# Performance work log

Hardware: AMD Instinct MI355X
Metric: run time of the kernel (lower is better)

The kernel has to match this reference:

```python
import jax, jax.numpy as jnp
import numpy as np

NUM_USERS = 1_000_000
EMBED_DIM = 64
N_NODES = 16384
K = 50
NEG_INF = -1e30


def setup_inputs() -> dict:
    key = jax.random.key(0)
    ks = jax.random.split(key, 7)
    d = EMBED_DIM
    table = jax.random.normal(ks[0], (NUM_USERS, d), jnp.float32) * 0.02
    nodes = jax.random.randint(ks[1], (N_NODES,), 0, NUM_USERS)
    neigh_idx = jax.random.randint(ks[2], (N_NODES, K), 0, NUM_USERS)
    neigh_mask = jax.random.randint(ks[3], (N_NODES, K), 0, 2).astype(bool)
    neigh_mask = neigh_mask.at[:, 0].set(True)  # every node has >=1 neighbor
    W1 = jax.random.normal(ks[4], (2 * d, d), jnp.float32) / np.sqrt(2 * d)
    b1 = jnp.zeros((d,), jnp.float32)
    W2 = jax.random.normal(ks[5], (d, d), jnp.float32) / np.sqrt(d)
    b2 = jnp.zeros((d,), jnp.float32)
    W3 = jax.random.normal(ks[6], (d, 1), jnp.float32) / np.sqrt(d)
    b3 = jnp.zeros((1,), jnp.float32)
    return dict(table=table, W1=W1, b1=b1, W2=W2, b2=b2, W3=W3, b3=b3,
                nodes=nodes, neigh_idx=neigh_idx, neigh_mask=neigh_mask)


def reference(table, W1, b1, W2, b2, W3, b3, nodes, neigh_idx, neigh_mask):
    # Gather neighbor embeddings and center-node embeddings (eval mode: dropout off).
    E = table[neigh_idx]                                   # [N, K, d]
    U = table[nodes]                                       # [N, d]
    Uk = jnp.broadcast_to(U[:, None, :], E.shape)          # [N, K, d]
    x = jnp.concatenate([E, Uk], axis=-1)                  # [N, K, 2d]
    h = jax.nn.relu(x @ W1 + b1)                           # [N, K, d]
    h = jax.nn.relu(h @ W2 + b2)                           # [N, K, d]
    s = (h @ W3 + b3)[..., 0]                              # [N, K]
    # Masked softmax over the ragged neighbor dimension.
    s = jnp.where(neigh_mask, s, NEG_INF)
    att = jax.nn.softmax(s, axis=-1)                       # [N, K]
    # Attention-weighted sum of neighbor embeddings: e_u.T @ att_w per node.
    out = jnp.einsum('nk,nkd->nd', att, E)                 # [N, d]
    return out
```

## Files before the change

### kernel.cpp

```cpp
#include <hip/hip_runtime.h>
#include <hip/hip_bf16.h>

#define NN 16384
#define KK 50
#define DD 64

typedef __attribute__((ext_vector_type(8))) short bf16x8;
typedef __attribute__((ext_vector_type(4))) float f32x4;

__device__ __forceinline__ float bf2f(unsigned short u) {
    union { unsigned int i; float f; } v;
    v.i = ((unsigned int)u) << 16;
    return v.f;
}
__device__ __forceinline__ unsigned short f2bf(float f) {
    union { float f; unsigned int i; } v; v.f = f;
    unsigned int lsb = (v.i >> 16) & 1u;
    v.i += 0x7fffu + lsb;
    return (unsigned short)(v.i >> 16);
}

template<int BF16>
__device__ __forceinline__ float ldv(const void* p, size_t i) {
    if (BF16) return bf2f(((const unsigned short*)p)[i]);
    else      return ((const float*)p)[i];
}

template<int BF16>
__device__ __forceinline__ bf16x8 load8(const void* p, size_t off) {
    if (BF16) {
        return *(const bf16x8*)((const unsigned short*)p + off);
    } else {
        const float* f = (const float*)p + off;
        bf16x8 r;
#pragma unroll
        for (int j = 0; j < 8; ++j) ((unsigned short*)&r)[j] = f2bf(f[j]);
        return r;
    }
}

__global__ void prep_kernel(const unsigned int* __restrict__ tw,
                            const unsigned int* __restrict__ mw,
                            const void* __restrict__ W1_,
                            const void* __restrict__ W2_,
                            int* __restrict__ flags,
                            unsigned short* __restrict__ W1top,
                            unsigned short* __restrict__ W1bot,
                            unsigned short* __restrict__ W2p) {
    __shared__ int sflags[2];
    const int t = threadIdx.x;
    if (t < 64) {
        const unsigned int w  = tw[t];
        const unsigned int lo = w & 0xFFFFu;
        const unsigned int ex = (lo >> 7) & 0xFFu;
        const bool bf_like = (ex >= 96u && ex <= 126u);
        const unsigned long long bb = __ballot(bf_like);
        bool found = false;
#pragma unroll
        for (int i = 0; i < 8; ++i) found |= (mw[t + i * 64] > 1u);
        const unsigned long long mb = __ballot(found);
        if (t == 0) {
            sflags[0] = (mb != 0ull) ? 1 : 0;
            sflags[1] = (__popcll(bb) >= 48) ? 1 : 0;
            flags[0] = sflags[0];
            flags[1] = sflags[1];
        }
    }
    __syncthreads();
    const int bf = sflags[1];
    {
        const int f = t >> 6, lane = t & 63;
        const int kt = f >> 2, nt = f & 3;
        const int q = lane >> 4, col = lane & 15;
#pragma unroll
        for (int j = 0; j < 8; ++j) {
            const int k = kt * 32 + q * 8 + j;
            const int n = nt * 16 + col;
            const float v = bf ? bf2f(((const unsigned short*)W1_)[k * 64 + n])
                               : ((const float*)W1_)[k * 64 + n];
            unsigned short* dst = (kt < 2) ? W1top : W1bot;
            const int fl = ((kt & 1) * 4 + nt);
            dst[((size_t)fl * 64 + lane) * 8 + j] = f2bf(v);
        }
    }
    if (t < 512) {
        const int f = t >> 6, lane = t & 63;
        const int kt = f >> 2, nt = f & 3;
        const int q = lane >> 4, col = lane & 15;
#pragma unroll
        for (int j = 0; j < 8; ++j) {
            const int k = kt * 32 + q * 8 + j;
            const int n = nt * 16 + col;
            const float v = bf ? bf2f(((const unsigned short*)W2_)[k * 64 + n])
                               : ((const float*)W2_)[k * 64 + n];
            W2p[((size_t)f * 64 + lane) * 8 + j] = f2bf(v);
        }
    }
}

template<int BF16>
__device__ __forceinline__ void uw_impl(
    const void* __restrict__ table_, const void* __restrict__ b1_,
    const int* __restrict__ nodes,
    const unsigned short* __restrict__ W1bot,
    float* __restrict__ UW)
{
    const int wave = threadIdx.x >> 6;
    const int lane = threadIdx.x & 63;
    const int q    = lane >> 4;
    const int col  = lane & 15;
    const int base = (blockIdx.x * 4 + wave) * 64;

    bf16x8 afrag[4][2];
#pragma unroll
    for (int mt = 0; mt < 4; ++mt) {
        const size_t row = (size_t)nodes[base + mt * 16 + col];
#pragma unroll
        for (int kt = 0; kt < 2; ++kt)
            afrag[mt][kt] = load8<BF16>(table_, row * 64 + kt * 32 + q * 8);
    }

    f32x4 acc[4][4];
#pragma unroll
    for (int mt = 0; mt < 4; ++mt)
#pragma unroll
        for (int nt = 0; nt < 4; ++nt) acc[mt][nt] = (f32x4){0.f, 0.f, 0.f, 0.f};

#pragma unroll
    for (int kt = 0; kt < 2; ++kt)
#pragma unroll
        for (int nt = 0; nt < 4; ++nt) {
            const bf16x8 b = *(const bf16x8*)(W1bot + ((size_t)(kt * 4 + nt) * 64 + lane) * 8);
#pragma unroll
            for (int mt = 0; mt < 4; ++mt)
                acc[mt][nt] = __builtin_amdgcn_mfma_f32_16x16x32_bf16(afrag[mt][kt], b, acc[mt][nt], 0, 0, 0);
        }

    float b1v[4];
#pragma unroll
    for (int nt = 0; nt < 4; ++nt) b1v[nt] = ldv<BF16>(b1_, nt * 16 + col);
#pragma unroll
    for (int mt = 0; mt < 4; ++mt)
#pragma unroll
        for (int nt = 0; nt < 4; ++nt)
#pragma unroll
            for (int r = 0; r < 4; ++r)
                UW[(size_t)(base + mt * 16 + q * 4 + r) * 64 + nt * 16 + col] =
                    acc[mt][nt][r] + b1v[nt];
}

__global__ __launch_bounds__(256) void uw_kernel(
    const void* __restrict__ table_, const void* __restrict__ b1_,
    const int* __restrict__ nodes, const int* __restrict__ flags,
    const unsigned short* __restrict__ W1bot, float* __restrict__ UW)
{
    if (flags[1]) uw_impl<1>(table_, b1_, nodes, W1bot, UW);
    else          uw_impl<0>(table_, b1_, nodes, W1bot, UW);
}

template<int BF16>
__device__ __forceinline__ void agg_impl(
    const void* __restrict__ table_,
    const void* __restrict__ b2_, const void* __restrict__ W3_,
    const int*  __restrict__ nodes,
    const int*  __restrict__ neigh_idx,
    const void* __restrict__ neigh_mask,
    int mu8,
    const unsigned short* __restrict__ W1top,
    const unsigned short* __restrict__ W2p,
    const float* __restrict__ UW,
    unsigned short* __restrict__ h1,
    float* __restrict__ scr,
    void* __restrict__ out_)
{
    const int wave = threadIdx.x >> 6;
    const int lane = threadIdx.x & 63;
    const int n    = blockIdx.x * 2 + wave;
    const int q    = lane >> 4;
    const int col  = lane & 15;

    int  rowidx [4];
    bool rowmask[4];
#pragma unroll
    for (int mt = 0; mt < 4; ++mt) {
        const int k = mt * 16 + col;
        bool mk = false; int idx = 0;
        if (k < KK) {
            mk = mu8 ? (((const unsigned char*)neigh_mask)[(size_t)n * KK + k] != 0)
                     : (((const int*)neigh_mask)[(size_t)n * KK + k] != 0);
            if (mk) idx = neigh_idx[(size_t)n * KK + k];
        }
        rowidx[mt] = idx; rowmask[mt] = mk;
    }

    bf16x8 afrag[4][2];
#pragma unroll
    for (int mt = 0; mt < 4; ++mt)
#pragma unroll
        for (int kt = 0; kt < 2; ++kt)
            afrag[mt][kt] = load8<BF16>(table_, (size_t)rowidx[mt] * 64 + kt * 32 + q * 8);

    float uwv[4];
#pragma unroll
    for (int nt = 0; nt < 4; ++nt) uwv[nt] = UW[(size_t)n * 64 + nt * 16 + col];

    f32x4 acc1[4][4];
#pragma unroll
    for (int mt = 0; mt < 4; ++mt)
#pragma unroll
        for (int nt = 0; nt < 4; ++nt) acc1[mt][nt] = (f32x4){0.f, 0.f, 0.f, 0.f};

#pragma unroll
    for (int kt = 0; kt < 2; ++kt)
#pragma unroll
        for (int nt = 0; nt < 4; ++nt) {
            const bf16x8 b = *(const bf16x8*)(W1top + ((size_t)(kt * 4 + nt) * 64 + lane) * 8);
#pragma unroll
            for (int mt = 0; mt < 4; ++mt)
                acc1[mt][nt] = __builtin_amdgcn_mfma_f32_16x16x32_bf16(afrag[mt][kt], b, acc1[mt][nt], 0, 0, 0);
        }

#pragma unroll
    for (int mt = 0; mt < 4; ++mt)
#pragma unroll
        for (int nt = 0; nt < 4; ++nt)
#pragma unroll
            for (int r = 0; r < 4; ++r) {
                const float v = fmaxf(acc1[mt][nt][r] + uwv[nt], 0.f);
                h1[(mt * 16 + q * 4 + r) * 72 + nt * 16 + col] = f2bf(v);
            }
    __builtin_amdgcn_wave_barrier();

    f32x4 acc2[4][4];
#pragma unroll
    for (int mt = 0; mt < 4; ++mt)
#pragma unroll
        for (int nt = 0; nt < 4; ++nt) acc2[mt][nt] = (f32x4){0.f, 0.f, 0.f, 0.f};

#pragma unroll
    for (int kt = 0; kt < 2; ++kt) {
        bf16x8 a2[4];
#pragma unroll
        for (int mt = 0; mt < 4; ++mt)
            a2[mt] = *(const bf16x8*)&h1[(mt * 16 + col) * 72 + kt * 32 + q * 8];
#pragma unroll
        for (int nt = 0; nt < 4; ++nt) {
            const bf16x8 b = *(const bf16x8*)(W2p + ((size_t)(kt * 4 + nt) * 64 + lane) * 8);
#pragma unroll
            for (int mt = 0; mt < 4; ++mt)
                acc2[mt][nt] = __builtin_amdgcn_mfma_f32_16x16x32_bf16(a2[mt], b, acc2[mt][nt], 0, 0, 0);
        }
    }

    float b2v[4], w3v[4];
#pragma unroll
    for (int nt = 0; nt < 4; ++nt) {
        b2v[nt] = ldv<BF16>(b2_, nt * 16 + col);
        w3v[nt] = ldv<BF16>(W3_, nt * 16 + col);
    }

    float s[4][4];
#pragma unroll
    for (int mt = 0; mt < 4; ++mt) {
        const unsigned long long bm = __ballot(rowmask[mt]);
#pragma unroll
        for (int r = 0; r < 4; ++r) {
            float p = 0.f;
#pragma unroll
            for (int nt = 0; nt < 4; ++nt)
                p += fmaxf(acc2[mt][nt][r] + b2v[nt], 0.f) * w3v[nt];
            p += __shfl_xor(p, 1, 64);
            p += __shfl_xor(p, 2, 64);
            p += __shfl_xor(p, 4, 64);
            p += __shfl_xor(p, 8, 64);
            const bool mk = (bm >> (q * 4 + r)) & 1ull;
            s[mt][r] = mk ? p : -1.0e30f;
        }
    }

    float mx = -3.0e38f;
#pragma unroll
    for (int mt = 0; mt < 4; ++mt)
#pragma unroll
        for (int r = 0; r < 4; ++r) mx = fmaxf(mx, s[mt][r]);
    mx = fmaxf(mx, __shfl_xor(mx, 16, 64));
    mx = fmaxf(mx, __shfl_xor(mx, 32, 64));

    float e[4][4], lsum = 0.f;
#pragma unroll
    for (int mt = 0; mt < 4; ++mt)
#pragma unroll
        for (int r = 0; r < 4; ++r) {
            e[mt][r] = expf(s[mt][r] - mx);
            lsum += e[mt][r];
        }
    lsum += __shfl_xor(lsum, 16, 64);
    lsum += __shfl_xor(lsum, 32, 64);
    const float inv = 1.f / lsum;

    if (col == 0)
#pragma unroll
        for (int mt = 0; mt < 4; ++mt)
#pragma unroll
            for (int r = 0; r < 4; ++r)
                scr[mt * 16 + q * 4 + r] = e[mt][r] * inv;
    __builtin_amdgcn_wave_barrier();

    float attr[4];
#pragma unroll
    for (int mt = 0; mt < 4; ++mt) attr[mt] = scr[mt * 16 + col];

    float v[2][8];
#pragma unroll
    for (int kt = 0; kt < 2; ++kt)
#pragma unroll
        for (int j = 0; j < 8; ++j) v[kt][j] = 0.f;
#pragma unroll
    for (int mt = 0; mt < 4; ++mt)
#pragma unroll
        for (int kt = 0; kt < 2; ++kt)
#pragma unroll
            for (int j = 0; j < 8; ++j)
                v[kt][j] += attr[mt] * bf2f(((const unsigned short*)&afrag[mt][kt])[j]);

#pragma unroll
    for (int off = 1; off <= 8; off <<= 1)
#pragma unroll
        for (int kt = 0; kt < 2; ++kt)
#pragma unroll
            for (int j = 0; j < 8; ++j)
                v[kt][j] += __shfl_xor(v[kt][j], off, 64);

    __builtin_amdgcn_wave_barrier();
    if (col == 0)
#pragma unroll
        for (int kt = 0; kt < 2; ++kt)
#pragma unroll
            for (int j = 0; j < 8; ++j)
                scr[kt * 32 + q * 8 + j] = v[kt][j];
    __builtin_amdgcn_wave_barrier();

    const float res = scr[lane];
    if (BF16) ((unsigned short*)out_)[(size_t)n * 64 + lane] = f2bf(res);
    else      ((float*)out_)[(size_t)n * 64 + lane] = res;
}

__global__ __launch_bounds__(128) void agg_kernel(
    const void* __restrict__ table_,
    const void* __restrict__ b2_, const void* __restrict__ W3_,
    const int*  __restrict__ nodes,
    const int*  __restrict__ neigh_idx,
    const void* __restrict__ neigh_mask,
    const int*  __restrict__ flags,
    const unsigned short* __restrict__ W1top,
    const unsigned short* __restrict__ W2p,
    const float* __restrict__ UW,
    void* __restrict__ out_)
{
    __shared__ unsigned short h1_sh[2][64][72];
    __shared__ float scr_sh[2][64];
    const int wave = threadIdx.x >> 6;
    if (flags[1])
        agg_impl<1>(table_, b2_, W3_, nodes, neigh_idx, neigh_mask, flags[0],
                    W1top, W2p, UW, &h1_sh[wave][0][0], &scr_sh[wave][0], out_);
    else
        agg_impl<0>(table_, b2_, W3_, nodes, neigh_idx, neigh_mask, flags[0],
                    W1top, W2p, UW, &h1_sh[wave][0][0], &scr_sh[wave][0], out_);
}

extern "C" void kernel_launch(void* const* d_in, const int* in_sizes, int n_in,
                              void* d_out, int out_size, void* d_ws, size_t ws_size,
                              hipStream_t stream) {
    const void* table = d_in[0];
    const void* W1    = d_in[1];
    const void* b1    = d_in[2];
    const void* W2    = d_in[3];
    const void* b2    = d_in[4];
    const void* W3    = d_in[5];
    const void* b3    = d_in[6]; (void)b3;
    const int*  nodes = (const int*)d_in[7];
    const int*  nidx  = (const int*)d_in[8];
    const void* nmask = d_in[9];

    char* ws = (char*)d_ws;
    int* flags            = (int*)ws;
    unsigned short* W1top = (unsigned short*)(ws + 1024);
    unsigned short* W1bot = (unsigned short*)(ws + 1024 + 8192);
    unsigned short* W2p   = (unsigned short*)(ws + 1024 + 16384);
    float* UW             = (float*)(ws + 32768);

    prep_kernel<<<1, 1024, 0, stream>>>((const unsigned int*)table,
                                        (const unsigned int*)nmask,
                                        W1, W2, flags, W1top, W1bot, W2p);
    uw_kernel<<<NN / 256, 256, 0, stream>>>(table, b1, nodes, flags, W1bot, UW);
    agg_kernel<<<NN / 2, 128, 0, stream>>>(table, b2, W3, nodes, nidx, nmask,
                                           flags, W1top, W2p, UW, d_out);
}
```

Baseline: 410.2 us.

## Transpose MFMA operands in agg kernel to keep scores per-row and shrink accumulators

```diff
diff --git a/kernel.cpp b/kernel.cpp
--- a/kernel.cpp
+++ b/kernel.cpp
@@ -19,11 +19,26 @@
     v.i += 0x7fffu + lsb;
     return (unsigned short)(v.i >> 16);
 }
+__device__ __forceinline__ unsigned int pk2bf(float lo, float hi) {
+    unsigned int w;
+    asm("v_cvt_pk_bf16_f32 %0, %1, %2" : "=v"(w) : "v"(lo), "v"(hi));
+    return w;
+}
 
 template<int BF16>
 __device__ __forceinline__ float ldv(const void* p, size_t i) {
     if (BF16) return bf2f(((const unsigned short*)p)[i]);
     else      return ((const float*)p)[i];
+}
+
+template<int BF16>
+__device__ __forceinline__ f32x4 ld4(const void* p, size_t i) {
+    if (BF16) {
+        const ushort4 u = *(const ushort4*)((const unsigned short*)p + i);
+        return (f32x4){bf2f(u.x), bf2f(u.y), bf2f(u.z), bf2f(u.w)};
+    } else {
+        return *(const f32x4*)((const float*)p + i);
+    }
 }
 
 template<int BF16>
@@ -32,10 +47,14 @@
         return *(const bf16x8*)((const unsigned short*)p + off);
     } else {
         const float* f = (const float*)p + off;
-        bf16x8 r;
-#pragma unroll
-        for (int j = 0; j < 8; ++j) ((unsigned short*)&r)[j] = f2bf(f[j]);
-        return r;
+        const f32x4 a = *(const f32x4*)f;
+        const f32x4 b = *(const f32x4*)(f + 4);
+        union { bf16x8 v; unsigned int w[4]; } r;
+        r.w[0] = pk2bf(a[0], a[1]);
+        r.w[1] = pk2bf(a[2], a[3]);
+        r.w[2] = pk2bf(b[0], b[1]);
+        r.w[3] = pk2bf(b[2], b[3]);
+        return r.v;
     }
 }
 
@@ -162,7 +181,6 @@
 __device__ __forceinline__ void agg_impl(
     const void* __restrict__ table_,
     const void* __restrict__ b2_, const void* __restrict__ W3_,
-    const int*  __restrict__ nodes,
     const int*  __restrict__ neigh_idx,
     const void* __restrict__ neigh_mask,
     int mu8,
@@ -173,9 +191,8 @@
     float* __restrict__ scr,
     void* __restrict__ out_)
 {
-    const int wave = threadIdx.x >> 6;
     const int lane = threadIdx.x & 63;
-    const int n    = blockIdx.x * 2 + wave;
+    const int n    = blockIdx.x * 2 + (threadIdx.x >> 6);
     const int q    = lane >> 4;
     const int col  = lane & 15;
 
@@ -183,14 +200,14 @@
     bool rowmask[4];
 #pragma unroll
     for (int mt = 0; mt < 4; ++mt) {
-        const int k = mt * 16 + col;
-        bool mk = false; int idx = 0;
-        if (k < KK) {
-            mk = mu8 ? (((const unsigned char*)neigh_mask)[(size_t)n * KK + k] != 0)
-                     : (((const int*)neigh_mask)[(size_t)n * KK + k] != 0);
-            if (mk) idx = neigh_idx[(size_t)n * KK + k];
-        }
-        rowidx[mt] = idx; rowmask[mt] = mk;
+        const int k  = mt * 16 + col;
+        const int kc = (k < KK) ? k : (KK - 1);
+        const int ir = neigh_idx[(size_t)n * KK + kc];
+        bool mk = mu8 ? (((const unsigned char*)neigh_mask)[(size_t)n * KK + kc] != 0)
+                      : (((const int*)neigh_mask)[(size_t)n * KK + kc] != 0);
+        mk = mk && (k < KK);
+        rowmask[mt] = mk;
+        rowidx[mt]  = mk ? ir : 0;
     }
 
     bf16x8 afrag[4][2];
@@ -200,120 +217,99 @@
         for (int kt = 0; kt < 2; ++kt)
             afrag[mt][kt] = load8<BF16>(table_, (size_t)rowidx[mt] * 64 + kt * 32 + q * 8);
 
-    float uwv[4];
-#pragma unroll
-    for (int nt = 0; nt < 4; ++nt) uwv[nt] = UW[(size_t)n * 64 + nt * 16 + col];
-
-    f32x4 acc1[4][4];
-#pragma unroll
-    for (int mt = 0; mt < 4; ++mt)
-#pragma unroll
-        for (int nt = 0; nt < 4; ++nt) acc1[mt][nt] = (f32x4){0.f, 0.f, 0.f, 0.f};
-
+#pragma unroll
+    for (int ct = 0; ct < 4; ++ct) {
+        const bf16x8 wA0 = *(const bf16x8*)(W1top + ((size_t)(0 * 4 + ct) * 64 + lane) * 8);
+        const bf16x8 wA1 = *(const bf16x8*)(W1top + ((size_t)(1 * 4 + ct) * 64 + lane) * 8);
+        f32x4 acc[4];
+#pragma unroll
+        for (int mt = 0; mt < 4; ++mt) acc[mt] = (f32x4){0.f, 0.f, 0.f, 0.f};
+#pragma unroll
+        for (int mt = 0; mt < 4; ++mt)
+            acc[mt] = __builtin_amdgcn_mfma_f32_16x16x32_bf16(wA0, afrag[mt][0], acc[mt], 0, 0, 0);
+#pragma unroll
+        for (int mt = 0; mt < 4; ++mt)
+            acc[mt] = __builtin_amdgcn_mfma_f32_16x16x32_bf16(wA1, afrag[mt][1], acc[mt], 0, 0, 0);
+
+        const f32x4 uw4 = *(const f32x4*)&UW[(size_t)n * 64 + ct * 16 + q * 4];
+#pragma unroll
+        for (int mt = 0; mt < 4; ++mt) {
+            const float h0 = fmaxf(acc[mt][0] + uw4[0], 0.f);
+            const float hv1 = fmaxf(acc[mt][1] + uw4[1], 0.f);
+            const float h2 = fmaxf(acc[mt][2] + uw4[2], 0.f);
+            const float h3 = fmaxf(acc[mt][3] + uw4[3], 0.f);
+            uint2 w;
+            w.x = pk2bf(h0, hv1);
+            w.y = pk2bf(h2, h3);
+            *(uint2*)&h1[(size_t)(mt * 16 + col) * 72 + ct * 16 + q * 4] = w;
+        }
+    }
+    __builtin_amdgcn_wave_barrier();
+
+    bf16x8 bfrag[4][2];
+#pragma unroll
+    for (int mt = 0; mt < 4; ++mt)
+#pragma unroll
+        for (int kt = 0; kt < 2; ++kt)
+            bfrag[mt][kt] = *(const bf16x8*)&h1[(size_t)(mt * 16 + col) * 72 + kt * 32 + q * 8];
+
+    float p[4] = {0.f, 0.f, 0.f, 0.f};
+#pragma unroll
+    for (int ct = 0; ct < 4; ++ct) {
+        const bf16x8 wB0 = *(const bf16x8*)(W2p + ((size_t)(0 * 4 + ct) * 64 + lane) * 8);
+        const bf16x8 wB1 = *(const bf16x8*)(W2p + ((size_t)(1 * 4 + ct) * 64 + lane) * 8);
+        f32x4 acc[4];
+#pragma unroll
+        for (int mt = 0; mt < 4; ++mt) acc[mt] = (f32x4){0.f, 0.f, 0.f, 0.f};
+#pragma unroll
+        for (int mt = 0; mt < 4; ++mt)
+            acc[mt] = __builtin_amdgcn_mfma_f32_16x16x32_bf16(wB0, bfrag[mt][0], acc[mt], 0, 0, 0);
+#pragma unroll
+        for (int mt = 0; mt < 4; ++mt)
+            acc[mt] = __builtin_amdgcn_mfma_f32_16x16x32_bf16(wB1, bfrag[mt][1], acc[mt], 0, 0, 0);
+
+        const f32x4 b2v = ld4<BF16>(b2_, ct * 16 + q * 4);
+        const f32x4 w3v = ld4<BF16>(W3_, ct * 16 + q * 4);
+#pragma unroll
+        for (int mt = 0; mt < 4; ++mt) {
+            float t = 0.f;
+#pragma unroll
+            for (int r = 0; r < 4; ++r)
+                t += fmaxf(acc[mt][r] + b2v[r], 0.f) * w3v[r];
+            p[mt] += t;
+        }
+    }
+
+#pragma unroll
+    for (int mt = 0; mt < 4; ++mt) {
+        p[mt] += __shfl_xor(p[mt], 16, 64);
+        p[mt] += __shfl_xor(p[mt], 32, 64);
+        if (!rowmask[mt]) p[mt] = -1.0e30f;
+    }
+
+    float mx = fmaxf(fmaxf(p[0], p[1]), fmaxf(p[2], p[3]));
+    mx = fmaxf(mx, __shfl_xor(mx, 1, 64));
+    mx = fmaxf(mx, __shfl_xor(mx, 2, 64));
+    mx = fmaxf(mx, __shfl_xor(mx, 4, 64));
+    mx = fmaxf(mx, __shfl_xor(mx, 8, 64));
+
+    float e[4], ls = 0.f;
+#pragma unroll
+    for (int mt = 0; mt < 4; ++mt) { e[mt] = __expf(p[mt] - mx); ls += e[mt]; }
+    ls += __shfl_xor(ls, 1, 64);
+    ls += __shfl_xor(ls, 2, 64);
+    ls += __shfl_xor(ls, 4, 64);
+    ls += __shfl_xor(ls, 8, 64);
+    const float inv = 1.f / ls;
+
+    float att[4];
+#pragma unroll
+    for (int mt = 0; mt < 4; ++mt) att[mt] = e[mt] * inv;
+
+    float v[2][8];
 #pragma unroll
     for (int kt = 0; kt < 2; ++kt)
 #pragma unroll
-        for (int nt = 0; nt < 4; ++nt) {
-            const bf16x8 b = *(const bf16x8*)(W1top + ((size_t)(kt * 4 + nt) * 64 + lane) * 8);
-#pragma unroll
-            for (int mt = 0; mt < 4; ++mt)
-                acc1[mt][nt] = __builtin_amdgcn_mfma_f32_16x16x32_bf16(afrag[mt][kt], b, acc1[mt][nt], 0, 0, 0);
-        }
-
-#pragma unroll
-    for (int mt = 0; mt < 4; ++mt)
-#pragma unroll
-        for (int nt = 0; nt < 4; ++nt)
-#pragma unroll
-            for (int r = 0; r < 4; ++r) {
-                const float v = fmaxf(acc1[mt][nt][r] + uwv[nt], 0.f);
-                h1[(mt * 16 + q * 4 + r) * 72 + nt * 16 + col] = f2bf(v);
-            }
-    __builtin_amdgcn_wave_barrier();
-
-    f32x4 acc2[4][4];
-#pragma unroll
-    for (int mt = 0; mt < 4; ++mt)
-#pragma unroll
-        for (int nt = 0; nt < 4; ++nt) acc2[mt][nt] = (f32x4){0.f, 0.f, 0.f, 0.f};
-
-#pragma unroll
-    for (int kt = 0; kt < 2; ++kt) {
-        bf16x8 a2[4];
-#pragma unroll
-        for (int mt = 0; mt < 4; ++mt)
-            a2[mt] = *(const bf16x8*)&h1[(mt * 16 + col) * 72 + kt * 32 + q * 8];
-#pragma unroll
-        for (int nt = 0; nt < 4; ++nt) {
-            const bf16x8 b = *(const bf16x8*)(W2p + ((size_t)(kt * 4 + nt) * 64 + lane) * 8);
-#pragma unroll
-            for (int mt = 0; mt < 4; ++mt)
-                acc2[mt][nt] = __builtin_amdgcn_mfma_f32_16x16x32_bf16(a2[mt], b, acc2[mt][nt], 0, 0, 0);
-        }
-    }
-
-    float b2v[4], w3v[4];
-#pragma unroll
-    for (int nt = 0; nt < 4; ++nt) {
-        b2v[nt] = ldv<BF16>(b2_, nt * 16 + col);
-        w3v[nt] = ldv<BF16>(W3_, nt * 16 + col);
-    }
-
-    float s[4][4];
-#pragma unroll
-    for (int mt = 0; mt < 4; ++mt) {
-        const unsigned long long bm = __ballot(rowmask[mt]);
-#pragma unroll
-        for (int r = 0; r < 4; ++r) {
-            float p = 0.f;
-#pragma unroll
-            for (int nt = 0; nt < 4; ++nt)
-                p += fmaxf(acc2[mt][nt][r] + b2v[nt], 0.f) * w3v[nt];
-            p += __shfl_xor(p, 1, 64);
-            p += __shfl_xor(p, 2, 64);
-            p += __shfl_xor(p, 4, 64);
-            p += __shfl_xor(p, 8, 64);
-            const bool mk = (bm >> (q * 4 + r)) & 1ull;
-            s[mt][r] = mk ? p : -1.0e30f;
-        }
-    }
-
-    float mx = -3.0e38f;
-#pragma unroll
-    for (int mt = 0; mt < 4; ++mt)
-#pragma unroll
-        for (int r = 0; r < 4; ++r) mx = fmaxf(mx, s[mt][r]);
-    mx = fmaxf(mx, __shfl_xor(mx, 16, 64));
-    mx = fmaxf(mx, __shfl_xor(mx, 32, 64));
-
-    float e[4][4], lsum = 0.f;
-#pragma unroll
-    for (int mt = 0; mt < 4; ++mt)
-#pragma unroll
-        for (int r = 0; r < 4; ++r) {
-            e[mt][r] = expf(s[mt][r] - mx);
-            lsum += e[mt][r];
-        }
-    lsum += __shfl_xor(lsum, 16, 64);
-    lsum += __shfl_xor(lsum, 32, 64);
-    const float inv = 1.f / lsum;
-
-    if (col == 0)
-#pragma unroll
-        for (int mt = 0; mt < 4; ++mt)
-#pragma unroll
-            for (int r = 0; r < 4; ++r)
-                scr[mt * 16 + q * 4 + r] = e[mt][r] * inv;
-    __builtin_amdgcn_wave_barrier();
-
-    float attr[4];
-#pragma unroll
-    for (int mt = 0; mt < 4; ++mt) attr[mt] = scr[mt * 16 + col];
-
-    float v[2][8];
-#pragma unroll
-    for (int kt = 0; kt < 2; ++kt)
-#pragma unroll
         for (int j = 0; j < 8; ++j) v[kt][j] = 0.f;
 #pragma unroll
     for (int mt = 0; mt < 4; ++mt)
@@ -321,7 +317,7 @@
         for (int kt = 0; kt < 2; ++kt)
 #pragma unroll
             for (int j = 0; j < 8; ++j)
-                v[kt][j] += attr[mt] * bf2f(((const unsigned short*)&afrag[mt][kt])[j]);
+                v[kt][j] += att[mt] * bf2f(((const unsigned short*)&afrag[mt][kt])[j]);
 
 #pragma unroll
     for (int off = 1; off <= 8; off <<= 1)
@@ -331,13 +327,13 @@
             for (int j = 0; j < 8; ++j)
                 v[kt][j] += __shfl_xor(v[kt][j], off, 64);
 
-    __builtin_amdgcn_wave_barrier();
-    if (col == 0)
-#pragma unroll
-        for (int kt = 0; kt < 2; ++kt)
-#pragma unroll
-            for (int j = 0; j < 8; ++j)
-                scr[kt * 32 + q * 8 + j] = v[kt][j];
+    if (col == 0) {
+#pragma unroll
+        for (int kt = 0; kt < 2; ++kt) {
+            *(f32x4*)&scr[kt * 32 + q * 8]     = (f32x4){v[kt][0], v[kt][1], v[kt][2], v[kt][3]};
+            *(f32x4*)&scr[kt * 32 + q * 8 + 4] = (f32x4){v[kt][4], v[kt][5], v[kt][6], v[kt][7]};
+        }
+    }
     __builtin_amdgcn_wave_barrier();
 
     const float res = scr[lane];
@@ -345,10 +341,9 @@
     else      ((float*)out_)[(size_t)n * 64 + lane] = res;
 }
 
-__global__ __launch_bounds__(128) void agg_kernel(
+__global__ __launch_bounds__(128, 4) void agg_kernel(
     const void* __restrict__ table_,
     const void* __restrict__ b2_, const void* __restrict__ W3_,
-    const int*  __restrict__ nodes,
     const int*  __restrict__ neigh_idx,
     const void* __restrict__ neigh_mask,
     const int*  __restrict__ flags,
@@ -361,10 +356,10 @@
     __shared__ float scr_sh[2][64];
     const int wave = threadIdx.x >> 6;
     if (flags[1])
-        agg_impl<1>(table_, b2_, W3_, nodes, neigh_idx, neigh_mask, flags[0],
+        agg_impl<1>(table_, b2_, W3_, neigh_idx, neigh_mask, flags[0],
                     W1top, W2p, UW, &h1_sh[wave][0][0], &scr_sh[wave][0], out_);
     else
-        agg_impl<0>(table_, b2_, W3_, nodes, neigh_idx, neigh_mask, flags[0],
+        agg_impl<0>(table_, b2_, W3_, neigh_idx, neigh_mask, flags[0],
                     W1top, W2p, UW, &h1_sh[wave][0][0], &scr_sh[wave][0], out_);
 }
 
@@ -393,6 +388,6 @@
                                         (const unsigned int*)nmask,
                                         W1, W2, flags, W1top, W1bot, W2p);
     uw_kernel<<<NN / 256, 256, 0, stream>>>(table, b1, nodes, flags, W1bot, UW);
-    agg_kernel<<<NN / 2, 128, 0, stream>>>(table, b2, W3, nodes, nidx, nmask,
+    agg_kernel<<<NN / 2, 128, 0, stream>>>(table, b2, W3, nidx, nmask,
                                            flags, W1top, W2p, UW, d_out);
 }
```

Result: faster. 379.2 us (-7.6%).
